# Performance work log

Hardware: AMD Instinct MI355X
Metric: run time of the kernel (lower is better)

## Reference

```python
import jax, jax.numpy as jnp
import numpy as np

# Irrep layout: 512x0e + 512x1o + 512x2e  (dims 512*1, 512*3, 512*5)
MUL = 512
LS = (0, 1, 2)


def setup_inputs() -> dict:
    key = jax.random.key(0)
    k1, k2, k3, k4 = jax.random.split(key, 4)
    N = 16384
    dim = MUL * sum(2 * l + 1 for l in LS)  # 4608
    x1 = jax.random.normal(k1, (N, dim), dtype=jnp.float32)
    x2 = jnp.ones((N, 1), dtype=jnp.float32)  # trivial 1x0e input of e3nn Linear
    W0 = jax.random.normal(k2, (MUL, 1, MUL), dtype=jnp.float32)
    W1 = jax.random.normal(k3, (MUL, 1, MUL), dtype=jnp.float32)
    W2 = jax.random.normal(k4, (MUL, 1, MUL), dtype=jnp.float32)
    return {"x1": x1, "x2": x2, "W0": W0, "W1": W1, "W2": W2}


def reference(x1, x2, W0, W1, W2):
    N = x1.shape[0]
    # path normalization: c = sqrt(alpha * path_weight / (mul_1 * mul_2)),
    # alpha = 1 (single path per output, unit variances), mul_2 = 1
    c = 1.0 / jnp.sqrt(jnp.asarray(MUL, dtype=x1.dtype))
    parts = []
    off = 0
    for W, l in ((W0, 0), (W1, 1), (W2, 2)):
        d = 2 * l + 1
        s1 = x1[:, off:off + MUL * d].reshape(N, MUL, d)  # [N, u, i]
        # specialized codegen branch (l2=0, l1=l_out, uvw):
        # out = c * einsum('uvw,zui,zv->zwi', ws, s1, s2)
        y = c * jnp.einsum('uvw,zui,zv->zwi', W, s1, x2)  # [N, w, i]
        parts.append(y.reshape(N, MUL * d))
        off += MUL * d
    return jnp.concatenate(parts, axis=1)
```

## Files before the change

kernel.cpp:

```cpp
#include <hip/hip_runtime.h>
#include <stdint.h>

typedef float f32x4 __attribute__((ext_vector_type(4)));
typedef __bf16 bf16x8 __attribute__((ext_vector_type(8)));
typedef unsigned short ushort4v __attribute__((ext_vector_type(4)));

#define DIM 4608
#define BK 32
#define NT 16
#define WS_L_BYTES (16 * 4 * 512 * 16)

#define BAR()                                    \
  do {                                           \
    __builtin_amdgcn_sched_barrier(0);           \
    asm volatile("s_waitcnt lgkmcnt(0)");        \
    __builtin_amdgcn_s_barrier();                \
    __builtin_amdgcn_sched_barrier(0);           \
  } while (0)

__global__ __launch_bounds__(256) void prepack(const float* __restrict__ W0,
                                               const float* __restrict__ W1,
                                               const float* __restrict__ W2,
                                               char* __restrict__ ws) {
  int gid = blockIdx.x * 256 + threadIdx.x;
  int col = gid & 511;
  int rest = gid >> 9;
  int grp = rest & 3;
  rest >>= 2;
  int t = rest & 15;
  int l = rest >> 4;
  const float* W = (l == 0) ? W0 : ((l == 1) ? W1 : W2);
  const float c = 0.044194173824159216f;
  union {
    bf16x8 v;
    uint4 u;
  } pk;
#pragma unroll
  for (int jj = 0; jj < 8; ++jj) {
    float v = W[(t * 32 + grp * 8 + jj) * 512 + col] * c;
    pk.v[jj] = (__bf16)v;
  }
  *(uint4*)(ws + (size_t)l * WS_L_BYTES + ((size_t)((t * 4 + grp) * 512 + col) << 4)) = pk.u;
}

template <int D, int BZ, int OFF>
__device__ __forceinline__ void gemm_body(int lb, const float* __restrict__ x1,
                                          const float* __restrict__ x2,
                                          const char* __restrict__ wsl,
                                          float* __restrict__ out,
                                          char* __restrict__ smem) {
  constexpr int BM = BZ * D;
  constexpr int R = BM / 16;
  constexpr int ABYTES = BM * 64;
  constexpr int CNT = BZ * 8 * D;
  constexpr int PF = (CNT + 511) / 512;

  const int tid = threadIdx.x;
  const int z0 = (lb >> 1) * BZ;
  const int cb = (lb & 1) * 256;
  const float* xbase = x1 + (size_t)z0 * DIM + OFF;

  const int lane = tid & 63;
  const int wave = tid >> 6;
  const int llo = lane & 15;
  const int lhi = lane >> 4;

  f32x4 acc[R][2];
#pragma unroll
  for (int rt = 0; rt < R; ++rt)
#pragma unroll
    for (int ct = 0; ct < 2; ++ct) acc[rt][ct] = (f32x4){0.f, 0.f, 0.f, 0.f};

  auto load_a = [&](f32x4 (&pa)[PF], int t) {
    const float* xs = xbase + t * (BK * D);
#pragma unroll
    for (int s = 0; s < PF; ++s) {
      int idx = tid + s * 512;
      if (idx < CNT) {
        int zl = idx / (8 * D);
        int q = idx - zl * (8 * D);
        pa[s] = *(const f32x4*)(xs + (size_t)zl * DIM + q * 4);
      }
    }
  };

  auto load_b = [&](bf16x8 (&b)[2], int t) {
    const char* wt = wsl + (size_t)t * 32768;
#pragma unroll
    for (int ct = 0; ct < 2; ++ct)
      b[ct] = *(const bf16x8*)(wt + ((lhi * 512 + cb + wave * 32 + ct * 16 + llo) << 4));
  };

  auto stage_write = [&](char* buf, f32x4 (&pa)[PF]) {
#pragma unroll
    for (int s = 0; s < PF; ++s) {
      int idx = tid + s * 512;
      if (idx < CNT) {
        int zl = idx / (8 * D);
        int q = idx - zl * (8 * D);
        if (D == 1) {
          int u0 = q * 4;
          union {
            ushort4v us;
            __bf16 b[4];
          } pk;
#pragma unroll
          for (int e = 0; e < 4; ++e) pk.b[e] = (__bf16)pa[s][e];
          *(ushort4v*)(buf + ((u0 >> 3) * BM + zl) * 16 + (u0 & 7) * 2) = pk.us;
        } else {
#pragma unroll
          for (int e = 0; e < 4; ++e) {
            int cl = q * 4 + e;
            int u = cl / D;
            int i = cl - u * D;
            int r = zl * D + i;
            *(__bf16*)(buf + ((u >> 3) * BM + r) * 16 + (u & 7) * 2) = (__bf16)pa[s][e];
          }
        }
      }
    }
  };

  auto compute = [&](const char* buf, bf16x8 (&b)[2]) {
#pragma unroll
    for (int rt = 0; rt < R; ++rt) {
      bf16x8 af = *(const bf16x8*)(buf + ((lhi * BM + rt * 16 + llo) << 4));
#pragma unroll
      for (int ct = 0; ct < 2; ++ct)
        acc[rt][ct] = __builtin_amdgcn_mfma_f32_16x16x32_bf16(af, b[ct], acc[rt][ct], 0, 0, 0);
    }
  };

  f32x4 paE[PF], paO[PF];
  bf16x8 bE[2], bO[2];
  load_a(paE, 0);
  load_b(bE, 0);
  load_a(paO, 1);
  load_b(bO, 1);
  stage_write(smem, paE);
  load_a(paE, 2);
  BAR();

#pragma unroll
  for (int tt = 0; tt < NT / 2; ++tt) {
    const int t = 2 * tt;
    compute(smem, bE);
    if (t + 2 < NT) load_b(bE, t + 2);
    stage_write(smem + ABYTES, paO);
    if (t + 3 < NT) load_a(paO, t + 3);
    BAR();
    compute(smem + ABYTES, bO);
    if (t + 3 < NT) load_b(bO, t + 3);
    if (t + 2 < NT) {
      stage_write(smem, paE);
      if (t + 4 < NT) load_a(paE, t + 4);
      BAR();
    }
  }

  float* obase = out + (size_t)z0 * DIM + OFF;
#pragma unroll
  for (int rt = 0; rt < R; ++rt) {
#pragma unroll
    for (int reg = 0; reg < 4; ++reg) {
      int row = rt * 16 + lhi * 4 + reg;
      int z = row / D;
      int i = row - z * D;
      float s = x2[z0 + z];
#pragma unroll
      for (int ct = 0; ct < 2; ++ct) {
        int col = cb + wave * 32 + ct * 16 + llo;
        obase[(size_t)z * DIM + col * D + i] = acc[rt][ct][reg] * s;
      }
    }
  }
}

__global__ __launch_bounds__(512, 4) void gemm_fused(const float* __restrict__ x1,
                                                     const float* __restrict__ x2,
                                                     const char* __restrict__ ws,
                                                     float* __restrict__ out) {
  __shared__ __align__(16) char smem[10240];
  int bid = blockIdx.x;
  if (bid < 2048) {
    gemm_body<5, 16, 2048>(bid, x1, x2, ws + 2 * (size_t)WS_L_BYTES, out, smem);
  } else if (bid < 4096) {
    gemm_body<3, 16, 512>(bid - 2048, x1, x2, ws + (size_t)WS_L_BYTES, out, smem);
  } else {
    gemm_body<1, 64, 0>(bid - 4096, x1, x2, ws, out, smem);
  }
}

extern "C" void kernel_launch(void* const* d_in, const int* in_sizes, int n_in,
                              void* d_out, int out_size, void* d_ws, size_t ws_size,
                              hipStream_t stream) {
  const float* x1 = (const float*)d_in[0];
  const float* x2 = (const float*)d_in[1];
  const float* W0 = (const float*)d_in[2];
  const float* W1 = (const float*)d_in[3];
  const float* W2 = (const float*)d_in[4];
  float* out = (float*)d_out;
  char* ws = (char*)d_ws;

  prepack<<<384, 256, 0, stream>>>(W0, W1, W2, ws);
  gemm_fused<<<4608, 512, 0, stream>>>(x1, x2, ws, out);
}
```

Measured before the change: 229.9 us.

## Narrow column tiles to 128, double K step, and swizzle block order

```diff
diff --git a/kernel.cpp b/kernel.cpp
--- a/kernel.cpp
+++ b/kernel.cpp
@@ -6,8 +6,8 @@
 typedef unsigned short ushort4v __attribute__((ext_vector_type(4)));
 
 #define DIM 4608
-#define BK 32
-#define NT 16
+#define BK 64
+#define NT 8
 #define WS_L_BYTES (16 * 4 * 512 * 16)
 
 #define BAR()                                    \
@@ -44,20 +44,20 @@
 }
 
 template <int D, int BZ, int OFF>
-__device__ __forceinline__ void gemm_body(int lb, const float* __restrict__ x1,
+__device__ __forceinline__ void gemm_body(int c, int j, const float* __restrict__ x1,
                                           const float* __restrict__ x2,
                                           const char* __restrict__ wsl,
                                           float* __restrict__ out,
                                           char* __restrict__ smem) {
   constexpr int BM = BZ * D;
   constexpr int R = BM / 16;
-  constexpr int ABYTES = BM * 64;
-  constexpr int CNT = BZ * 8 * D;
+  constexpr int ABYTES = BM * BK * 2;
+  constexpr int CNT = BZ * 16 * D;
   constexpr int PF = (CNT + 511) / 512;
 
   const int tid = threadIdx.x;
-  const int z0 = (lb >> 1) * BZ;
-  const int cb = (lb & 1) * 256;
+  const int z0 = c * BZ;
+  const int cb = j * 128;
   const float* xbase = x1 + (size_t)z0 * DIM + OFF;
 
   const int lane = tid & 63;
@@ -65,56 +65,59 @@
   const int llo = lane & 15;
   const int lhi = lane >> 4;
 
-  f32x4 acc[R][2];
-#pragma unroll
-  for (int rt = 0; rt < R; ++rt)
-#pragma unroll
-    for (int ct = 0; ct < 2; ++ct) acc[rt][ct] = (f32x4){0.f, 0.f, 0.f, 0.f};
+  f32x4 acc[R];
+#pragma unroll
+  for (int rt = 0; rt < R; ++rt) acc[rt] = (f32x4){0.f, 0.f, 0.f, 0.f};
 
   auto load_a = [&](f32x4 (&pa)[PF], int t) {
     const float* xs = xbase + t * (BK * D);
 #pragma unroll
     for (int s = 0; s < PF; ++s) {
       int idx = tid + s * 512;
-      if (idx < CNT) {
-        int zl = idx / (8 * D);
-        int q = idx - zl * (8 * D);
+      if ((CNT % 512 == 0) || idx < CNT) {
+        int zl = idx / (16 * D);
+        int q = idx - zl * (16 * D);
         pa[s] = *(const f32x4*)(xs + (size_t)zl * DIM + q * 4);
       }
     }
   };
 
   auto load_b = [&](bf16x8 (&b)[2], int t) {
-    const char* wt = wsl + (size_t)t * 32768;
-#pragma unroll
-    for (int ct = 0; ct < 2; ++ct)
-      b[ct] = *(const bf16x8*)(wt + ((lhi * 512 + cb + wave * 32 + ct * 16 + llo) << 4));
+#pragma unroll
+    for (int kk = 0; kk < 2; ++kk)
+      b[kk] = *(const bf16x8*)(wsl + (size_t)(2 * t + kk) * 32768 +
+                               ((lhi * 512 + cb + wave * 16 + llo) << 4));
   };
 
   auto stage_write = [&](char* buf, f32x4 (&pa)[PF]) {
 #pragma unroll
     for (int s = 0; s < PF; ++s) {
       int idx = tid + s * 512;
-      if (idx < CNT) {
-        int zl = idx / (8 * D);
-        int q = idx - zl * (8 * D);
+      if ((CNT % 512 == 0) || idx < CNT) {
+        int zl = idx / (16 * D);
+        int q = idx - zl * (16 * D);
         if (D == 1) {
           int u0 = q * 4;
+          int kk = u0 >> 5;
+          int ul = u0 & 31;
           union {
             ushort4v us;
             __bf16 b[4];
           } pk;
 #pragma unroll
           for (int e = 0; e < 4; ++e) pk.b[e] = (__bf16)pa[s][e];
-          *(ushort4v*)(buf + ((u0 >> 3) * BM + zl) * 16 + (u0 & 7) * 2) = pk.us;
+          *(ushort4v*)(buf + kk * (BM * 64) + ((ul >> 3) * BM + zl) * 16 + (ul & 7) * 2) = pk.us;
         } else {
 #pragma unroll
           for (int e = 0; e < 4; ++e) {
             int cl = q * 4 + e;
             int u = cl / D;
             int i = cl - u * D;
+            int kk = u >> 5;
+            int ul = u & 31;
             int r = zl * D + i;
-            *(__bf16*)(buf + ((u >> 3) * BM + r) * 16 + (u & 7) * 2) = (__bf16)pa[s][e];
+            *(__bf16*)(buf + kk * (BM * 64) + ((ul >> 3) * BM + r) * 16 + (ul & 7) * 2) =
+                (__bf16)pa[s][e];
           }
         }
       }
@@ -123,11 +126,12 @@
 
   auto compute = [&](const char* buf, bf16x8 (&b)[2]) {
 #pragma unroll
-    for (int rt = 0; rt < R; ++rt) {
-      bf16x8 af = *(const bf16x8*)(buf + ((lhi * BM + rt * 16 + llo) << 4));
-#pragma unroll
-      for (int ct = 0; ct < 2; ++ct)
-        acc[rt][ct] = __builtin_amdgcn_mfma_f32_16x16x32_bf16(af, b[ct], acc[rt][ct], 0, 0, 0);
+    for (int kk = 0; kk < 2; ++kk) {
+#pragma unroll
+      for (int rt = 0; rt < R; ++rt) {
+        bf16x8 af = *(const bf16x8*)(buf + kk * (BM * 64) + ((lhi * BM + rt * 16 + llo) << 4));
+        acc[rt] = __builtin_amdgcn_mfma_f32_16x16x32_bf16(af, b[kk], acc[rt], 0, 0, 0);
+      }
     }
   };
 
@@ -167,27 +171,33 @@
       int z = row / D;
       int i = row - z * D;
       float s = x2[z0 + z];
-#pragma unroll
-      for (int ct = 0; ct < 2; ++ct) {
-        int col = cb + wave * 32 + ct * 16 + llo;
-        obase[(size_t)z * DIM + col * D + i] = acc[rt][ct][reg] * s;
-      }
-    }
-  }
-}
-
-__global__ __launch_bounds__(512, 4) void gemm_fused(const float* __restrict__ x1,
+      int col = cb + wave * 16 + llo;
+      obase[(size_t)z * DIM + col * D + i] = acc[rt][reg] * s;
+    }
+  }
+}
+
+__global__ __launch_bounds__(512, 6) void gemm_fused(const float* __restrict__ x1,
                                                      const float* __restrict__ x2,
                                                      const char* __restrict__ ws,
                                                      float* __restrict__ out) {
-  __shared__ __align__(16) char smem[10240];
+  __shared__ __align__(16) char smem[20480];
   int bid = blockIdx.x;
-  if (bid < 2048) {
-    gemm_body<5, 16, 2048>(bid, x1, x2, ws + 2 * (size_t)WS_L_BYTES, out, smem);
-  } else if (bid < 4096) {
-    gemm_body<3, 16, 512>(bid - 2048, x1, x2, ws + (size_t)WS_L_BYTES, out, smem);
+  if (bid < 4096) {
+    int b = bid;
+    int c = (b & 7) + 8 * (b >> 5);
+    int j = (b >> 3) & 3;
+    gemm_body<5, 16, 2048>(c, j, x1, x2, ws + 2 * (size_t)WS_L_BYTES, out, smem);
+  } else if (bid < 8192) {
+    int b = bid - 4096;
+    int c = (b & 7) + 8 * (b >> 5);
+    int j = (b >> 3) & 3;
+    gemm_body<3, 16, 512>(c, j, x1, x2, ws + (size_t)WS_L_BYTES, out, smem);
   } else {
-    gemm_body<1, 64, 0>(bid - 4096, x1, x2, ws, out, smem);
+    int b = bid - 8192;
+    int c = (b & 7) + 8 * (b >> 5);
+    int j = (b >> 3) & 3;
+    gemm_body<1, 64, 0>(c, j, x1, x2, ws, out, smem);
   }
 }
 
@@ -203,5 +213,5 @@
   char* ws = (char*)d_ws;
 
   prepack<<<384, 256, 0, stream>>>(W0, W1, W2, ws);
-  gemm_fused<<<4608, 512, 0, stream>>>(x1, x2, ws, out);
-}
+  gemm_fused<<<9216, 512, 0, stream>>>(x1, x2, ws, out);
+}
```

Measured after the change: 496.4 us. 116% more time.

## Stage A tiles via direct global-to-LDS loads with in-LDS bf16 repack

Applied to the files above, without the earlier changes.

```diff
diff --git a/kernel.cpp b/kernel.cpp
--- a/kernel.cpp
+++ b/kernel.cpp
@@ -3,17 +3,16 @@
 
 typedef float f32x4 __attribute__((ext_vector_type(4)));
 typedef __bf16 bf16x8 __attribute__((ext_vector_type(8)));
-typedef unsigned short ushort4v __attribute__((ext_vector_type(4)));
 
 #define DIM 4608
-#define BK 32
-#define NT 16
+#define BK 64
+#define NT 8
 #define WS_L_BYTES (16 * 4 * 512 * 16)
 
-#define BAR()                                    \
+#define BARLGKM()                                \
   do {                                           \
     __builtin_amdgcn_sched_barrier(0);           \
-    asm volatile("s_waitcnt lgkmcnt(0)");        \
+    asm volatile("s_waitcnt lgkmcnt(0)" ::: "memory"); \
     __builtin_amdgcn_s_barrier();                \
     __builtin_amdgcn_sched_barrier(0);           \
   } while (0)
@@ -44,20 +43,26 @@
 }
 
 template <int D, int BZ, int OFF>
-__device__ __forceinline__ void gemm_body(int lb, const float* __restrict__ x1,
+__device__ __forceinline__ void gemm_body(int zc, int j, const float* __restrict__ x1,
                                           const float* __restrict__ x2,
                                           const char* __restrict__ wsl,
                                           float* __restrict__ out,
                                           char* __restrict__ smem) {
   constexpr int BM = BZ * D;
   constexpr int R = BM / 16;
-  constexpr int ABYTES = BM * 64;
-  constexpr int CNT = BZ * 8 * D;
-  constexpr int PF = (CNT + 511) / 512;
+  constexpr int RAWB = BZ * BK * D * 4;
+  constexpr int CH = RAWB / 16;
+  constexpr int CPR = BK * D / 4;
+  constexpr int UNITS = BM * (BK / 8);
+  constexpr int KD = (CH + 511) / 512;
+  constexpr int KU = (UNITS + 511) / 512;
+
+  char* rawbuf = smem;
+  char* fragbuf = smem + 2 * RAWB;
 
   const int tid = threadIdx.x;
-  const int z0 = (lb >> 1) * BZ;
-  const int cb = (lb & 1) * 256;
+  const int z0 = zc * BZ;
+  const int cb = j * 256;
   const float* xbase = x1 + (size_t)z0 * DIM + OFF;
 
   const int lane = tid & 63;
@@ -65,97 +70,87 @@
   const int llo = lane & 15;
   const int lhi = lane >> 4;
 
+  const float* gsrc[KD];
+#pragma unroll
+  for (int k = 0; k < KD; ++k) {
+    int c = tid + k * 512;
+    int rowz = c / CPR;
+    int off = c - rowz * CPR;
+    gsrc[k] = xbase + (size_t)rowz * DIM + off * 4;
+  }
+
   f32x4 acc[R][2];
 #pragma unroll
   for (int rt = 0; rt < R; ++rt)
 #pragma unroll
     for (int ct = 0; ct < 2; ++ct) acc[rt][ct] = (f32x4){0.f, 0.f, 0.f, 0.f};
 
-  auto load_a = [&](f32x4 (&pa)[PF], int t) {
-    const float* xs = xbase + t * (BK * D);
-#pragma unroll
-    for (int s = 0; s < PF; ++s) {
-      int idx = tid + s * 512;
-      if (idx < CNT) {
-        int zl = idx / (8 * D);
-        int q = idx - zl * (8 * D);
-        pa[s] = *(const f32x4*)(xs + (size_t)zl * DIM + q * 4);
+  auto dma = [&](int t) {
+    char* ldst = rawbuf + (t & 1) * RAWB;
+    const int tof = t * (BK * D);
+#pragma unroll
+    for (int k = 0; k < KD; ++k) {
+      int c = tid + k * 512;
+      if ((CH % 512 == 0) || (c < CH)) {
+        __builtin_amdgcn_global_load_lds(
+            (const __attribute__((address_space(1))) uint32_t*)(gsrc[k] + tof),
+            (__attribute__((address_space(3))) uint32_t*)(ldst + (size_t)c * 16), 16, 0, 0);
       }
     }
   };
 
-  auto load_b = [&](bf16x8 (&b)[2], int t) {
-    const char* wt = wsl + (size_t)t * 32768;
-#pragma unroll
-    for (int ct = 0; ct < 2; ++ct)
-      b[ct] = *(const bf16x8*)(wt + ((lhi * 512 + cb + wave * 32 + ct * 16 + llo) << 4));
-  };
-
-  auto stage_write = [&](char* buf, f32x4 (&pa)[PF]) {
-#pragma unroll
-    for (int s = 0; s < PF; ++s) {
-      int idx = tid + s * 512;
-      if (idx < CNT) {
-        int zl = idx / (8 * D);
-        int q = idx - zl * (8 * D);
-        if (D == 1) {
-          int u0 = q * 4;
-          union {
-            ushort4v us;
-            __bf16 b[4];
-          } pk;
-#pragma unroll
-          for (int e = 0; e < 4; ++e) pk.b[e] = (__bf16)pa[s][e];
-          *(ushort4v*)(buf + ((u0 >> 3) * BM + zl) * 16 + (u0 & 7) * 2) = pk.us;
-        } else {
-#pragma unroll
-          for (int e = 0; e < 4; ++e) {
-            int cl = q * 4 + e;
-            int u = cl / D;
-            int i = cl - u * D;
-            int r = zl * D + i;
-            *(__bf16*)(buf + ((u >> 3) * BM + r) * 16 + (u & 7) * 2) = (__bf16)pa[s][e];
-          }
-        }
+  auto repack = [&](int t) {
+    const float* raw = (const float*)(rawbuf + (t & 1) * RAWB);
+#pragma unroll
+    for (int s = 0; s < KU; ++s) {
+      int u = tid + s * 512;
+      if ((UNITS % 512 == 0) || (u < UNITS)) {
+        int kg = u / BM;
+        int r = u - kg * BM;
+        int z = r / D;
+        int i = r - z * D;
+        const float* base = raw + z * (BK * D) + (kg * 8) * D + i;
+        bf16x8 v;
+#pragma unroll
+        for (int jj = 0; jj < 8; ++jj) v[jj] = (__bf16)base[jj * D];
+        *(bf16x8*)(fragbuf + (size_t)u * 16) = v;
       }
     }
   };
 
-  auto compute = [&](const char* buf, bf16x8 (&b)[2]) {
-#pragma unroll
-    for (int rt = 0; rt < R; ++rt) {
-      bf16x8 af = *(const bf16x8*)(buf + ((lhi * BM + rt * 16 + llo) << 4));
+  auto load_b = [&](bf16x8 (&b)[2][2], int t) {
+#pragma unroll
+    for (int kk = 0; kk < 2; ++kk)
 #pragma unroll
       for (int ct = 0; ct < 2; ++ct)
-        acc[rt][ct] = __builtin_amdgcn_mfma_f32_16x16x32_bf16(af, b[ct], acc[rt][ct], 0, 0, 0);
-    }
-  };
-
-  f32x4 paE[PF], paO[PF];
-  bf16x8 bE[2], bO[2];
-  load_a(paE, 0);
-  load_b(bE, 0);
-  load_a(paO, 1);
-  load_b(bO, 1);
-  stage_write(smem, paE);
-  load_a(paE, 2);
-  BAR();
-
-#pragma unroll
-  for (int tt = 0; tt < NT / 2; ++tt) {
-    const int t = 2 * tt;
-    compute(smem, bE);
-    if (t + 2 < NT) load_b(bE, t + 2);
-    stage_write(smem + ABYTES, paO);
-    if (t + 3 < NT) load_a(paO, t + 3);
-    BAR();
-    compute(smem + ABYTES, bO);
-    if (t + 3 < NT) load_b(bO, t + 3);
-    if (t + 2 < NT) {
-      stage_write(smem, paE);
-      if (t + 4 < NT) load_a(paE, t + 4);
-      BAR();
-    }
+        b[kk][ct] = *(const bf16x8*)(wsl + ((size_t)(((2 * t + kk) * 4 + lhi) * 512 + cb +
+                                                    wave * 32 + ct * 16 + llo)
+                                            << 4));
+  };
+
+  auto compute = [&](bf16x8 (&b)[2][2]) {
+#pragma unroll
+    for (int kk = 0; kk < 2; ++kk)
+#pragma unroll
+      for (int rt = 0; rt < R; ++rt) {
+        bf16x8 af =
+            *(const bf16x8*)(fragbuf + (((kk * 4 + lhi) * BM + rt * 16 + llo) << 4));
+#pragma unroll
+        for (int ct = 0; ct < 2; ++ct)
+          acc[rt][ct] = __builtin_amdgcn_mfma_f32_16x16x32_bf16(af, b[kk][ct], acc[rt][ct], 0, 0, 0);
+      }
+  };
+
+  dma(0);
+#pragma unroll 2
+  for (int t = 0; t < NT; ++t) {
+    __syncthreads();
+    if (t + 1 < NT) dma(t + 1);
+    bf16x8 b[2][2];
+    load_b(b, t);
+    repack(t);
+    BARLGKM();
+    compute(b);
   }
 
   float* obase = out + (size_t)z0 * DIM + OFF;
@@ -180,14 +175,16 @@
                                                      const float* __restrict__ x2,
                                                      const char* __restrict__ ws,
                                                      float* __restrict__ out) {
-  __shared__ __align__(16) char smem[10240];
+  __shared__ __align__(16) char smem[51200];
   int bid = blockIdx.x;
   if (bid < 2048) {
-    gemm_body<5, 16, 2048>(bid, x1, x2, ws + 2 * (size_t)WS_L_BYTES, out, smem);
+    gemm_body<5, 16, 2048>(bid >> 1, bid & 1, x1, x2, ws + 2 * (size_t)WS_L_BYTES, out, smem);
   } else if (bid < 4096) {
-    gemm_body<3, 16, 512>(bid - 2048, x1, x2, ws + (size_t)WS_L_BYTES, out, smem);
+    int b = bid - 2048;
+    gemm_body<3, 16, 512>(b >> 1, b & 1, x1, x2, ws + (size_t)WS_L_BYTES, out, smem);
   } else {
-    gemm_body<1, 64, 0>(bid - 4096, x1, x2, ws, out, smem);
+    int b = bid - 4096;
+    gemm_body<1, 64, 0>(b >> 1, b & 1, x1, x2, ws, out, smem);
   }
 }
 
```

New measurement: 235.2 us. +2.3%, slower.

## Give each wave a private LDS A tile and drop block barriers

Applied to the files above, without the earlier changes.

```diff
diff --git a/kernel.cpp b/kernel.cpp
--- a/kernel.cpp
+++ b/kernel.cpp
@@ -9,14 +9,6 @@
 #define BK 32
 #define NT 16
 #define WS_L_BYTES (16 * 4 * 512 * 16)
-
-#define BAR()                                    \
-  do {                                           \
-    __builtin_amdgcn_sched_barrier(0);           \
-    asm volatile("s_waitcnt lgkmcnt(0)");        \
-    __builtin_amdgcn_s_barrier();                \
-    __builtin_amdgcn_sched_barrier(0);           \
-  } while (0)
 
 __global__ __launch_bounds__(256) void prepack(const float* __restrict__ W0,
                                                const float* __restrict__ W1,
@@ -44,26 +36,27 @@
 }
 
 template <int D, int BZ, int OFF>
-__device__ __forceinline__ void gemm_body(int lb, const float* __restrict__ x1,
+__device__ __forceinline__ void gemm_body(int zc, int j, const float* __restrict__ x1,
                                           const float* __restrict__ x2,
                                           const char* __restrict__ wsl,
                                           float* __restrict__ out,
                                           char* __restrict__ smem) {
   constexpr int BM = BZ * D;
   constexpr int R = BM / 16;
-  constexpr int ABYTES = BM * 64;
-  constexpr int CNT = BZ * 8 * D;
-  constexpr int PF = (CNT + 511) / 512;
+  constexpr int WBYTES = BM * 64;
+  constexpr int PF = BZ * 8 * D / 64;
 
   const int tid = threadIdx.x;
-  const int z0 = (lb >> 1) * BZ;
-  const int cb = (lb & 1) * 256;
-  const float* xbase = x1 + (size_t)z0 * DIM + OFF;
-
   const int lane = tid & 63;
   const int wave = tid >> 6;
   const int llo = lane & 15;
   const int lhi = lane >> 4;
+
+  char* wbuf = smem + wave * WBYTES;
+
+  const int z0 = zc * BZ;
+  const int cb = j * 256;
+  const float* xbase = x1 + (size_t)z0 * DIM + OFF;
 
   f32x4 acc[R][2];
 #pragma unroll
@@ -71,92 +64,76 @@
 #pragma unroll
     for (int ct = 0; ct < 2; ++ct) acc[rt][ct] = (f32x4){0.f, 0.f, 0.f, 0.f};
 
-  auto load_a = [&](f32x4 (&pa)[PF], int t) {
+  f32x4 pa[PF];
+  bf16x8 b[2];
+
+  auto load_a = [&](int t) {
     const float* xs = xbase + t * (BK * D);
 #pragma unroll
     for (int s = 0; s < PF; ++s) {
-      int idx = tid + s * 512;
-      if (idx < CNT) {
-        int zl = idx / (8 * D);
-        int q = idx - zl * (8 * D);
-        pa[s] = *(const f32x4*)(xs + (size_t)zl * DIM + q * 4);
-      }
+      int idx = lane + s * 64;
+      int zl = idx / (8 * D);
+      int q = idx - zl * (8 * D);
+      pa[s] = *(const f32x4*)(xs + (size_t)zl * DIM + q * 4);
     }
   };
 
-  auto load_b = [&](bf16x8 (&b)[2], int t) {
+  auto load_b = [&](int t) {
     const char* wt = wsl + (size_t)t * 32768;
 #pragma unroll
     for (int ct = 0; ct < 2; ++ct)
       b[ct] = *(const bf16x8*)(wt + ((lhi * 512 + cb + wave * 32 + ct * 16 + llo) << 4));
   };
 
-  auto stage_write = [&](char* buf, f32x4 (&pa)[PF]) {
+  auto stage = [&]() {
 #pragma unroll
     for (int s = 0; s < PF; ++s) {
-      int idx = tid + s * 512;
-      if (idx < CNT) {
-        int zl = idx / (8 * D);
-        int q = idx - zl * (8 * D);
-        if (D == 1) {
-          int u0 = q * 4;
-          union {
-            ushort4v us;
-            __bf16 b[4];
-          } pk;
+      int idx = lane + s * 64;
+      int zl = idx / (8 * D);
+      int q = idx - zl * (8 * D);
+      if (D == 1) {
+        int u0 = q * 4;
+        union {
+          ushort4v us;
+          __bf16 b4[4];
+        } pk;
 #pragma unroll
-          for (int e = 0; e < 4; ++e) pk.b[e] = (__bf16)pa[s][e];
-          *(ushort4v*)(buf + ((u0 >> 3) * BM + zl) * 16 + (u0 & 7) * 2) = pk.us;
-        } else {
+        for (int e = 0; e < 4; ++e) pk.b4[e] = (__bf16)pa[s][e];
+        *(ushort4v*)(wbuf + ((u0 >> 3) * BM + zl) * 16 + (u0 & 7) * 2) = pk.us;
+      } else {
 #pragma unroll
-          for (int e = 0; e < 4; ++e) {
-            int cl = q * 4 + e;
-            int u = cl / D;
-            int i = cl - u * D;
-            int r = zl * D + i;
-            *(__bf16*)(buf + ((u >> 3) * BM + r) * 16 + (u & 7) * 2) = (__bf16)pa[s][e];
-          }
+        for (int e = 0; e < 4; ++e) {
+          int f = q * 4 + e;
+          int u = f / D;
+          int i = f - u * D;
+          int r = zl * D + i;
+          *(__bf16*)(wbuf + ((u >> 3) * BM + r) * 16 + (u & 7) * 2) = (__bf16)pa[s][e];
         }
       }
     }
   };
 
-  auto compute = [&](const char* buf, bf16x8 (&b)[2]) {
+  auto compute = [&]() {
 #pragma unroll
     for (int rt = 0; rt < R; ++rt) {
-      bf16x8 af = *(const bf16x8*)(buf + ((lhi * BM + rt * 16 + llo) << 4));
+      bf16x8 af = *(const bf16x8*)(wbuf + ((lhi * BM + rt * 16 + llo) << 4));
 #pragma unroll
       for (int ct = 0; ct < 2; ++ct)
         acc[rt][ct] = __builtin_amdgcn_mfma_f32_16x16x32_bf16(af, b[ct], acc[rt][ct], 0, 0, 0);
     }
   };
 
-  f32x4 paE[PF], paO[PF];
-  bf16x8 bE[2], bO[2];
-  load_a(paE, 0);
-  load_b(bE, 0);
-  load_a(paO, 1);
-  load_b(bO, 1);
-  stage_write(smem, paE);
-  load_a(paE, 2);
-  BAR();
-
-#pragma unroll
-  for (int tt = 0; tt < NT / 2; ++tt) {
-    const int t = 2 * tt;
-    compute(smem, bE);
-    if (t + 2 < NT) load_b(bE, t + 2);
-    stage_write(smem + ABYTES, paO);
-    if (t + 3 < NT) load_a(paO, t + 3);
-    BAR();
-    compute(smem + ABYTES, bO);
-    if (t + 3 < NT) load_b(bO, t + 3);
-    if (t + 2 < NT) {
-      stage_write(smem, paE);
-      if (t + 4 < NT) load_a(paE, t + 4);
-      BAR();
-    }
+  load_a(0);
+#pragma unroll 1
+  for (int t = 0; t < NT - 1; ++t) {
+    stage();
+    load_a(t + 1);
+    load_b(t);
+    compute();
   }
+  stage();
+  load_b(NT - 1);
+  compute();
 
   float* obase = out + (size_t)z0 * DIM + OFF;
 #pragma unroll
@@ -180,14 +157,16 @@
                                                      const float* __restrict__ x2,
                                                      const char* __restrict__ ws,
                                                      float* __restrict__ out) {
-  __shared__ __align__(16) char smem[10240];
+  __shared__ __align__(16) char smem[8 * 5120];
   int bid = blockIdx.x;
   if (bid < 2048) {
-    gemm_body<5, 16, 2048>(bid, x1, x2, ws + 2 * (size_t)WS_L_BYTES, out, smem);
+    gemm_body<5, 16, 2048>(bid >> 1, bid & 1, x1, x2, ws + 2 * (size_t)WS_L_BYTES, out, smem);
   } else if (bid < 4096) {
-    gemm_body<3, 16, 512>(bid - 2048, x1, x2, ws + (size_t)WS_L_BYTES, out, smem);
+    int b = bid - 2048;
+    gemm_body<3, 16, 512>(b >> 1, b & 1, x1, x2, ws + (size_t)WS_L_BYTES, out, smem);
   } else {
-    gemm_body<1, 64, 0>(bid - 4096, x1, x2, ws, out, smem);
+    int b = bid - 4096;
+    gemm_body<1, 16, 0>(b >> 1, b & 1, x1, x2, ws, out, smem);
   }
 }
 
@@ -203,5 +182,5 @@
   char* ws = (char*)d_ws;
 
   prepack<<<384, 256, 0, stream>>>(W0, W1, W2, ws);
-  gemm_fused<<<4608, 512, 0, stream>>>(x1, x2, ws, out);
+  gemm_fused<<<6144, 512, 0, stream>>>(x1, x2, ws, out);
 }
```

Measured after the change: 817.8 us. 3.56x slower.
